# Kernel tuning notes

Measured on AMD Instinct MI355X. Metric: run time of the kernel, lower is better.

The kernel has to match this reference:

```python
import jax, jax.numpy as jnp
import numpy as np

D = 512
SCALE = float(np.sqrt(D // 8))  # sqrt(d_k), d_k = d_model/num_heads = 64
EPS = 1e-5


def _ln(x, g, b):
    m = jnp.mean(x, axis=-1, keepdims=True)
    v = jnp.var(x, axis=-1, keepdims=True)
    return (x - m) * jax.lax.rsqrt(v + EPS) * g + b


def setup_inputs() -> dict:
    key = jax.random.key(0)
    ks = jax.random.split(key, 12)
    B, S = 512, 512
    w = lambda k, shp: jax.random.normal(k, shp, dtype=jnp.float32) * 0.02
    return {
        "sentiment_vec": jax.random.normal(ks[0], (B, D), dtype=jnp.float32),
        "price_sequence": jax.random.normal(ks[1], (B, S, D), dtype=jnp.float32),
        "Wq": w(ks[2], (D, D)), "bq": jnp.zeros((D,), jnp.float32),
        "Wk": w(ks[3], (D, D)), "bk": jnp.zeros((D,), jnp.float32),
        "Wv": w(ks[4], (D, D)), "bv": jnp.zeros((D,), jnp.float32),
        "Wo": w(ks[5], (D, D)), "bo": jnp.zeros((D,), jnp.float32),
        "Wg": w(ks[6], (2 * D, D)), "bg": jnp.zeros((D,), jnp.float32),
        "g_q": jnp.ones((D,), jnp.float32), "beta_q": jnp.zeros((D,), jnp.float32),
        "g_kv": jnp.ones((D,), jnp.float32), "beta_kv": jnp.zeros((D,), jnp.float32),
    }


def reference(sentiment_vec, price_sequence, Wq, bq, Wk, bk, Wv, bv, Wo, bo,
              Wg, bg, g_q, beta_q, g_kv, beta_kv):
    # LayerNorms (query is a single token per batch element)
    Q = _ln(sentiment_vec, g_q, beta_q)            # [B, D]
    KV = _ln(price_sequence, g_kv, beta_kv)        # [B, S, D]
    # Projections (note: forward never splits heads -> single-head attention)
    q = Q @ Wq + bq                                # [B, D]
    k = KV @ Wk + bk                               # [B, S, D]
    v = KV @ Wv + bv                               # [B, S, D]
    # Single-query attention
    scores = jnp.einsum('bd,bsd->bs', q, k) / SCALE
    attn = jax.nn.softmax(scores, axis=-1)         # [B, S] (dropout: eval mode)
    ctx = jnp.einsum('bs,bsd->bd', attn, v)        # [B, D]
    ctx = ctx @ Wo + bo
    # Sigmoid gate over concat([sentiment, context])
    gate_in = jnp.concatenate([sentiment_vec, ctx], axis=-1)  # [B, 2D]
    alpha = jax.nn.sigmoid(gate_in @ Wg + bg)
    fused = alpha * ctx + (1.0 - alpha) * sentiment_vec
    return fused, attn
```

## Files before the change

kernel.cpp:

```cpp
#include <hip/hip_runtime.h>

#define NB 512
#define NS 512
#define ND 512
#define INV_SCALE 0.125f
#define LN_EPS 1e-5f

typedef __attribute__((ext_vector_type(8))) short short8;
typedef __attribute__((ext_vector_type(4))) short short4v;
typedef __attribute__((ext_vector_type(4))) float float4v;

static __device__ __forceinline__ unsigned short f2bf(float x) {
    unsigned int u = __float_as_uint(x);
    unsigned int r = (u + 0x7fffu + ((u >> 16) & 1u)) >> 16;
    return (unsigned short)r;
}
static __device__ __forceinline__ float bf2f(unsigned short h) {
    return __uint_as_float(((unsigned int)h) << 16);
}

__global__ __launch_bounds__(256) void prep_k(
    const float* __restrict__ Wq, const float* __restrict__ Wk,
    const float* __restrict__ bq, const float* __restrict__ bk,
    const float* __restrict__ bv, const float* __restrict__ Wo,
    const float* __restrict__ bo,
    float* __restrict__ Wqk, float* __restrict__ wv,
    float* __restrict__ bqk, float* __restrict__ bvo, float* __restrict__ c0) {
    const int bid = blockIdx.x;
    const int t = threadIdx.x;
    const int wave = t >> 6, lane = t & 63;

    if (bid < 256) {
        constexpr int LDK = 40;
        __shared__ __align__(16) unsigned short Ah[32 * LDK];
        __shared__ __align__(16) unsigned short Al[32 * LDK];
        __shared__ __align__(16) unsigned short Bh[32 * LDK];
        __shared__ __align__(16) unsigned short Bl[32 * LDK];
        const int m0 = (bid >> 4) * 32, n0 = (bid & 15) * 32;
        const int wm = (wave & 1) * 16, wn = (wave >> 1) * 16;
        float4v acc = (float4v){0.f, 0.f, 0.f, 0.f};
        const int arow = wm + (lane & 15);
        const int brow = wn + (lane & 15);
        const int kq8 = (lane >> 4) * 8;
        const int srow = t >> 3, skq = (t & 7) * 4;

        float4 va = *(const float4*)(Wq + (size_t)(m0 + srow) * 512 + skq);
        float4 vb = *(const float4*)(Wk + (size_t)(n0 + srow) * 512 + skq);
        for (int k0 = 0; k0 < 512; k0 += 32) {
            {
                unsigned short h0 = f2bf(va.x), h1 = f2bf(va.y), h2 = f2bf(va.z), h3 = f2bf(va.w);
                short4v hv = {(short)h0, (short)h1, (short)h2, (short)h3};
                short4v lv = {(short)f2bf(va.x - bf2f(h0)), (short)f2bf(va.y - bf2f(h1)),
                              (short)f2bf(va.z - bf2f(h2)), (short)f2bf(va.w - bf2f(h3))};
                *(short4v*)&Ah[srow * LDK + skq] = hv;
                *(short4v*)&Al[srow * LDK + skq] = lv;
            }
            {
                unsigned short h0 = f2bf(vb.x), h1 = f2bf(vb.y), h2 = f2bf(vb.z), h3 = f2bf(vb.w);
                short4v hv = {(short)h0, (short)h1, (short)h2, (short)h3};
                short4v lv = {(short)f2bf(vb.x - bf2f(h0)), (short)f2bf(vb.y - bf2f(h1)),
                              (short)f2bf(vb.z - bf2f(h2)), (short)f2bf(vb.w - bf2f(h3))};
                *(short4v*)&Bh[srow * LDK + skq] = hv;
                *(short4v*)&Bl[srow * LDK + skq] = lv;
            }
            float4 va2, vb2;
            if (k0 + 32 < 512) {
                va2 = *(const float4*)(Wq + (size_t)(m0 + srow) * 512 + k0 + 32 + skq);
                vb2 = *(const float4*)(Wk + (size_t)(n0 + srow) * 512 + k0 + 32 + skq);
            } else { va2 = va; vb2 = vb; }
            __syncthreads();
            short8 ah = *(const short8*)&Ah[arow * LDK + kq8];
            short8 al = *(const short8*)&Al[arow * LDK + kq8];
            short8 bh = *(const short8*)&Bh[brow * LDK + kq8];
            short8 bl = *(const short8*)&Bl[brow * LDK + kq8];
            acc = __builtin_amdgcn_mfma_f32_16x16x32_bf16(ah, bh, acc, 0, 0, 0);
            acc = __builtin_amdgcn_mfma_f32_16x16x32_bf16(ah, bl, acc, 0, 0, 0);
            acc = __builtin_amdgcn_mfma_f32_16x16x32_bf16(al, bh, acc, 0, 0, 0);
            __syncthreads();
            va = va2; vb = vb2;
        }
        const int coln = lane & 15, rbase = (lane >> 4) * 4;
        const int n = n0 + wn + coln;
#pragma unroll
        for (int r = 0; r < 4; ++r)
            Wqk[(size_t)(m0 + wm + rbase + r) * 512 + n] = acc[r];
    } else if (bid == 256) {
        float4 k0v = *(const float4*)(bk + 4 * lane);
        float4 k1v = *(const float4*)(bk + 256 + 4 * lane);
        for (int m = wave; m < 512; m += 4) {
            const float* r = Wq + (size_t)m * 512;
            float4 a0 = *(const float4*)(r + 4 * lane);
            float4 a1 = *(const float4*)(r + 256 + 4 * lane);
            float d = a0.x * k0v.x + a0.y * k0v.y + a0.z * k0v.z + a0.w * k0v.w +
                      a1.x * k1v.x + a1.y * k1v.y + a1.z * k1v.z + a1.w * k1v.w;
            for (int off = 32; off; off >>= 1) d += __shfl_xor(d, off, 64);
            if (lane == 0) wv[m] = d;
        }
    } else if (bid == 257) {
        float4 q0v = *(const float4*)(bq + 4 * lane);
        float4 q1v = *(const float4*)(bq + 256 + 4 * lane);
        for (int n = wave; n < 512; n += 4) {
            const float* r = Wk + (size_t)n * 512;
            float4 a0 = *(const float4*)(r + 4 * lane);
            float4 a1 = *(const float4*)(r + 256 + 4 * lane);
            float d = a0.x * q0v.x + a0.y * q0v.y + a0.z * q0v.z + a0.w * q0v.w +
                      a1.x * q1v.x + a1.y * q1v.y + a1.z * q1v.z + a1.w * q1v.w;
            for (int off = 32; off; off >>= 1) d += __shfl_xor(d, off, 64);
            if (lane == 0) bqk[n] = d;
        }
        if (wave == 0) {
            float4 b0v = *(const float4*)(bk + 4 * lane);
            float4 b1v = *(const float4*)(bk + 256 + 4 * lane);
            float d = b0v.x * q0v.x + b0v.y * q0v.y + b0v.z * q0v.z + b0v.w * q0v.w +
                      b1v.x * q1v.x + b1v.y * q1v.y + b1v.z * q1v.z + b1v.w * q1v.w;
            for (int off = 32; off; off >>= 1) d += __shfl_xor(d, off, 64);
            if (lane == 0) c0[0] = d;
        }
    } else {
        float a0 = 0.f, a1 = 0.f;
#pragma unroll 4
        for (int k = 0; k < 512; ++k) {
            float s = bv[k];
            a0 = fmaf(s, Wo[(size_t)k * 512 + t], a0);
            a1 = fmaf(s, Wo[(size_t)k * 512 + 256 + t], a1);
        }
        bvo[t] = a0 + bo[t];
        bvo[t + 256] = a1 + bo[t + 256];
    }
}

__global__ __launch_bounds__(64) void ln_s0_k(const float* __restrict__ x,
                                              const float* __restrict__ g,
                                              const float* __restrict__ be,
                                              const float* __restrict__ wv,
                                              const float* __restrict__ c0,
                                              float* __restrict__ y,
                                              float* __restrict__ s0) {
    const int row = blockIdx.x;
    const int lane = threadIdx.x;
    const float* xr = x + (size_t)row * ND;
    float4 x0 = *(const float4*)(xr + 4 * lane);
    float4 x1 = *(const float4*)(xr + 256 + 4 * lane);
    float s1 = x0.x + x0.y + x0.z + x0.w + x1.x + x1.y + x1.z + x1.w;
    float s2 = x0.x * x0.x + x0.y * x0.y + x0.z * x0.z + x0.w * x0.w +
               x1.x * x1.x + x1.y * x1.y + x1.z * x1.z + x1.w * x1.w;
    for (int off = 32; off; off >>= 1) {
        s1 += __shfl_xor(s1, off, 64);
        s2 += __shfl_xor(s2, off, 64);
    }
    float mean = s1 * (1.f / 512.f);
    float rstd = rsqrtf(s2 * (1.f / 512.f) - mean * mean + LN_EPS);
    float4 g0 = *(const float4*)(g + 4 * lane);
    float4 g1 = *(const float4*)(g + 256 + 4 * lane);
    float4 b0 = *(const float4*)(be + 4 * lane);
    float4 b1 = *(const float4*)(be + 256 + 4 * lane);
    float4 y0, y1;
    y0.x = (x0.x - mean) * rstd * g0.x + b0.x;
    y0.y = (x0.y - mean) * rstd * g0.y + b0.y;
    y0.z = (x0.z - mean) * rstd * g0.z + b0.z;
    y0.w = (x0.w - mean) * rstd * g0.w + b0.w;
    y1.x = (x1.x - mean) * rstd * g1.x + b1.x;
    y1.y = (x1.y - mean) * rstd * g1.y + b1.y;
    y1.z = (x1.z - mean) * rstd * g1.z + b1.z;
    y1.w = (x1.w - mean) * rstd * g1.w + b1.w;
    float* yr = y + (size_t)row * ND;
    *(float4*)(yr + 4 * lane) = y0;
    *(float4*)(yr + 256 + 4 * lane) = y1;
    float4 w0 = *(const float4*)(wv + 4 * lane);
    float4 w1 = *(const float4*)(wv + 256 + 4 * lane);
    float d = y0.x * w0.x + y0.y * w0.y + y0.z * w0.z + y0.w * w0.w +
              y1.x * w1.x + y1.y * w1.y + y1.z * w1.z + y1.w * w1.w;
    for (int off = 32; off; off >>= 1) d += __shfl_xor(d, off, 64);
    if (lane == 0) s0[row] = d + c0[0];
}

template <int EPI>
__global__ __launch_bounds__(256) void gemm32_k(
    const float* __restrict__ A, const float* __restrict__ B,
    const float* __restrict__ bias, float* __restrict__ C, int N, int K,
    const float* __restrict__ e_ctx, const float* __restrict__ e_sent,
    const float* __restrict__ e_add) {
    constexpr int LDK = 40;
    __shared__ __align__(16) unsigned short Ah[32 * LDK];
    __shared__ __align__(16) unsigned short Al[32 * LDK];
    __shared__ __align__(16) unsigned short Bh[32 * LDK];
    __shared__ __align__(16) unsigned short Bl[32 * LDK];
    const int t = threadIdx.x;
    const int wave = t >> 6, lane = t & 63;
    const int m0 = blockIdx.y * 32, n0 = blockIdx.x * 32;
    const int wm = (wave & 1) * 16, wn = (wave >> 1) * 16;

    float4v acc = (float4v){0.f, 0.f, 0.f, 0.f};
    const int arow = wm + (lane & 15);
    const int brow = wn + (lane & 15);
    const int kq8 = (lane >> 4) * 8;
    const int srow = t >> 3, skq = (t & 7) * 4;

    float4 va = *(const float4*)(A + (size_t)(m0 + srow) * K + skq);
    float4 vb = *(const float4*)(B + (size_t)srow * N + n0 + skq);

    for (int k0 = 0; k0 < K; k0 += 32) {
        {
            unsigned short h0 = f2bf(va.x), h1 = f2bf(va.y), h2 = f2bf(va.z), h3 = f2bf(va.w);
            short4v hv = {(short)h0, (short)h1, (short)h2, (short)h3};
            short4v lv = {(short)f2bf(va.x - bf2f(h0)), (short)f2bf(va.y - bf2f(h1)),
                          (short)f2bf(va.z - bf2f(h2)), (short)f2bf(va.w - bf2f(h3))};
            *(short4v*)&Ah[srow * LDK + skq] = hv;
            *(short4v*)&Al[srow * LDK + skq] = lv;
        }
        {
            float vv[4] = {vb.x, vb.y, vb.z, vb.w};
#pragma unroll
            for (int j = 0; j < 4; ++j) {
                unsigned short hh = f2bf(vv[j]);
                Bh[(skq + j) * LDK + srow] = hh;
                Bl[(skq + j) * LDK + srow] = f2bf(vv[j] - bf2f(hh));
            }
        }
        float4 va2, vb2;
        if (k0 + 32 < K) {
            va2 = *(const float4*)(A + (size_t)(m0 + srow) * K + k0 + 32 + skq);
            vb2 = *(const float4*)(B + (size_t)(k0 + 32 + srow) * N + n0 + skq);
        } else { va2 = va; vb2 = vb; }
        __syncthreads();
        short8 ah = *(const short8*)&Ah[arow * LDK + kq8];
        short8 al = *(const short8*)&Al[arow * LDK + kq8];
        short8 bh = *(const short8*)&Bh[brow * LDK + kq8];
        short8 bl = *(const short8*)&Bl[brow * LDK + kq8];
        acc = __builtin_amdgcn_mfma_f32_16x16x32_bf16(ah, bh, acc, 0, 0, 0);
        acc = __builtin_amdgcn_mfma_f32_16x16x32_bf16(ah, bl, acc, 0, 0, 0);
        acc = __builtin_amdgcn_mfma_f32_16x16x32_bf16(al, bh, acc, 0, 0, 0);
        __syncthreads();
        va = va2; vb = vb2;
    }

    const int coln = lane & 15, rbase = (lane >> 4) * 4;
    const int n = n0 + wn + coln;
    const float bvv = bias ? bias[n] : 0.f;
#pragma unroll
    for (int r = 0; r < 4; ++r) {
        int m = m0 + wm + rbase + r;
        float val = acc[r] + bvv;
        if (EPI == 2) {
            float z = val + e_add[(size_t)m * N + n];
            float a = 1.f / (1.f + __expf(-z));
            float cx = e_ctx[(size_t)m * N + n];
            float sv = e_sent[(size_t)m * N + n];
            val = a * cx + (1.f - a) * sv;
        }
        C[(size_t)m * N + n] = val;
    }
}

__global__ __launch_bounds__(512) void flash_fused_k(
    const float* __restrict__ ps, const float* __restrict__ g,
    const float* __restrict__ be, const float* __restrict__ qp,
    const float* __restrict__ s0v, float* __restrict__ ctx_pre,
    float* __restrict__ attn,
    const float* __restrict__ Wv, const float* __restrict__ Wo,
    float* __restrict__ Wvo,
    const float* __restrict__ sent, const float* __restrict__ Wg,
    const float* __restrict__ bg, float* __restrict__ sentg) {
    union SMemU {
        struct { float zbuf[NS]; float ubuf[8][ND]; float lw[8]; float tw[8]; } fl;
        struct { unsigned short Ah[64 * 40]; unsigned short Al[64 * 40];
                 unsigned short Bh[32 * 40]; unsigned short Bl[32 * 40]; } gm;
    };
    __shared__ __align__(16) SMemU sm;
    const int bid = blockIdx.x;
    const int t = threadIdx.x;
    const int wave = t >> 6, lane = t & 63;

    if (bid < 512) {
        const int b = bid;
        const float* qb = qp + (size_t)b * ND;
        float4 q0 = *(const float4*)(qb + 4 * lane);
        float4 q1 = *(const float4*)(qb + 256 + 4 * lane);
        float4 g0 = *(const float4*)(g + 4 * lane);
        float4 g1 = *(const float4*)(g + 256 + 4 * lane);
        float4 b0 = *(const float4*)(be + 4 * lane);
        float4 b1 = *(const float4*)(be + 256 + 4 * lane);

        float4 qg0, qg1;
        qg0.x = g0.x * q0.x; qg0.y = g0.y * q0.y; qg0.z = g0.z * q0.z; qg0.w = g0.w * q0.w;
        qg1.x = g1.x * q1.x; qg1.y = g1.y * q1.y; qg1.z = g1.z * q1.z; qg1.w = g1.w * q1.w;
        float c1 = qg0.x + qg0.y + qg0.z + qg0.w + qg1.x + qg1.y + qg1.z + qg1.w;
        float c2 = b0.x * q0.x + b0.y * q0.y + b0.z * q0.z + b0.w * q0.w +
                   b1.x * q1.x + b1.y * q1.y + b1.z * q1.z + b1.w * q1.w;
        for (int off = 32; off; off >>= 1) {
            c1 += __shfl_xor(c1, off, 64);
            c2 += __shfl_xor(c2, off, 64);
        }
        const float K2 = INV_SCALE * (c2 + s0v[b]);
        const float C1 = c1;

        float l = 0.f, t1 = 0.f;
        float4 u0 = {0.f, 0.f, 0.f, 0.f}, u1 = {0.f, 0.f, 0.f, 0.f};

        const float* base = ps + ((size_t)b * NS + wave * 64) * ND + 4 * lane;
        float4 xa0 = *(const float4*)(base);
        float4 xa1 = *(const float4*)(base + 256);
        float4 xb0 = *(const float4*)(base + ND);
        float4 xb1 = *(const float4*)(base + ND + 256);

        for (int r = 0; r < 64; r += 2) {
            float4 ya0, ya1, yb0, yb1;
            if (r < 62) {
                const float* nb = base + (size_t)(r + 2) * ND;
                ya0 = *(const float4*)(nb);
                ya1 = *(const float4*)(nb + 256);
                yb0 = *(const float4*)(nb + ND);
                yb1 = *(const float4*)(nb + ND + 256);
            } else {
                ya0 = xa0; ya1 = xa1; yb0 = xb0; yb1 = xb1;
            }
            float sa1 = xa0.x + xa0.y + xa0.z + xa0.w + xa1.x + xa1.y + xa1.z + xa1.w;
            float sb1 = xb0.x + xb0.y + xb0.z + xb0.w + xb1.x + xb1.y + xb1.z + xb1.w;
            float sa2 = xa0.x * xa0.x + xa0.y * xa0.y + xa0.z * xa0.z + xa0.w * xa0.w +
                        xa1.x * xa1.x + xa1.y * xa1.y + xa1.z * xa1.z + xa1.w * xa1.w;
            float sb2 = xb0.x * xb0.x + xb0.y * xb0.y + xb0.z * xb0.z + xb0.w * xb0.w +
                        xb1.x * xb1.x + xb1.y * xb1.y + xb1.z * xb1.z + xb1.w * xb1.w;
            float sa3 = xa0.x * qg0.x + xa0.y * qg0.y + xa0.z * qg0.z + xa0.w * qg0.w +
                        xa1.x * qg1.x + xa1.y * qg1.y + xa1.z * qg1.z + xa1.w * qg1.w;
            float sb3 = xb0.x * qg0.x + xb0.y * qg0.y + xb0.z * qg0.z + xb0.w * qg0.w +
                        xb1.x * qg1.x + xb1.y * qg1.y + xb1.z * qg1.z + xb1.w * qg1.w;
            for (int off = 32; off; off >>= 1) {
                sa1 += __shfl_xor(sa1, off, 64);
                sb1 += __shfl_xor(sb1, off, 64);
                sa2 += __shfl_xor(sa2, off, 64);
                sb2 += __shfl_xor(sb2, off, 64);
                sa3 += __shfl_xor(sa3, off, 64);
                sb3 += __shfl_xor(sb3, off, 64);
            }
            float meana = sa1 * (1.f / 512.f), meanb = sb1 * (1.f / 512.f);
            float rstda = rsqrtf(sa2 * (1.f / 512.f) - meana * meana + LN_EPS);
            float rstdb = rsqrtf(sb2 * (1.f / 512.f) - meanb * meanb + LN_EPS);
            float za = INV_SCALE * rstda * (sa3 - meana * C1) + K2;
            float zb = INV_SCALE * rstdb * (sb3 - meanb * C1) + K2;
            float pa = __expf(za), pb = __expf(zb);
            l += pa + pb;
            float pra = pa * rstda, prb = pb * rstdb;
            t1 += pra * meana + prb * meanb;
            u0.x += pra * xa0.x + prb * xb0.x;
            u0.y += pra * xa0.y + prb * xb0.y;
            u0.z += pra * xa0.z + prb * xb0.z;
            u0.w += pra * xa0.w + prb * xb0.w;
            u1.x += pra * xa1.x + prb * xb1.x;
            u1.y += pra * xa1.y + prb * xb1.y;
            u1.z += pra * xa1.z + prb * xb1.z;
            u1.w += pra * xa1.w + prb * xb1.w;
            if (lane == 0) {
                sm.fl.zbuf[wave * 64 + r] = za;
                sm.fl.zbuf[wave * 64 + r + 1] = zb;
            }
            xa0 = ya0; xa1 = ya1; xb0 = yb0; xb1 = yb1;
        }

        *(float4*)&sm.fl.ubuf[wave][4 * lane] = u0;
        *(float4*)&sm.fl.ubuf[wave][256 + 4 * lane] = u1;
        if (lane == 0) { sm.fl.lw[wave] = l; sm.fl.tw[wave] = t1; }
        __syncthreads();

        float U = 0.f;
#pragma unroll
        for (int w = 0; w < 8; ++w) U += sm.fl.ubuf[w][t];
        float L = 0.f, T = 0.f;
#pragma unroll
        for (int w = 0; w < 8; ++w) { L += sm.fl.lw[w]; T += sm.fl.tw[w]; }
        float invL = 1.f / L;
        ctx_pre[(size_t)b * ND + t] = g[t] * (U - T) * invL + be[t];
        attn[(size_t)b * NS + t] = __expf(sm.fl.zbuf[t]) * invL;
    } else {
        constexpr int LDK = 40;
        int gb = bid - 512;
        const float* A; const float* B; const float* bias; float* C;
        if (gb < 128) { A = Wv; B = Wo; bias = nullptr; C = Wvo; }
        else { gb -= 128; A = sent; B = Wg; bias = bg; C = sentg; }
        const int m0 = (gb >> 4) * 64, n0 = (gb & 15) * 32;
        const int wm = (wave & 3) * 16, wn = (wave >> 2) * 16;
        float4v acc = (float4v){0.f, 0.f, 0.f, 0.f};
        const int arow = wm + (lane & 15);
        const int brow = wn + (lane & 15);
        const int kq8 = (lane >> 4) * 8;
        const int srow = t >> 3, skq = (t & 7) * 4;
        unsigned short* Ah = sm.gm.Ah;
        unsigned short* Al = sm.gm.Al;
        unsigned short* Bh = sm.gm.Bh;
        unsigned short* Bl = sm.gm.Bl;

        float4 va = *(const float4*)(A + (size_t)(m0 + srow) * 512 + skq);
        float4 vb = {0.f, 0.f, 0.f, 0.f};
        const int bkrow = t >> 3, bnq = (t & 7) * 4;
        if (t < 256) vb = *(const float4*)(B + (size_t)bkrow * 512 + n0 + bnq);

        for (int k0 = 0; k0 < 512; k0 += 32) {
            {
                unsigned short h0 = f2bf(va.x), h1 = f2bf(va.y), h2 = f2bf(va.z), h3 = f2bf(va.w);
                short4v hv = {(short)h0, (short)h1, (short)h2, (short)h3};
                short4v lv = {(short)f2bf(va.x - bf2f(h0)), (short)f2bf(va.y - bf2f(h1)),
                              (short)f2bf(va.z - bf2f(h2)), (short)f2bf(va.w - bf2f(h3))};
                *(short4v*)&Ah[srow * LDK + skq] = hv;
                *(short4v*)&Al[srow * LDK + skq] = lv;
            }
            if (t < 256) {
                float vv[4] = {vb.x, vb.y, vb.z, vb.w};
#pragma unroll
                for (int j = 0; j < 4; ++j) {
                    unsigned short hh = f2bf(vv[j]);
                    Bh[(bnq + j) * LDK + bkrow] = hh;
                    Bl[(bnq + j) * LDK + bkrow] = f2bf(vv[j] - bf2f(hh));
                }
            }
            float4 va2 = va, vb2 = vb;
            if (k0 + 32 < 512) {
                va2 = *(const float4*)(A + (size_t)(m0 + srow) * 512 + k0 + 32 + skq);
                if (t < 256) vb2 = *(const float4*)(B + (size_t)(k0 + 32 + bkrow) * 512 + n0 + bnq);
            }
            __syncthreads();
            short8 ah = *(const short8*)&Ah[arow * LDK + kq8];
            short8 al = *(const short8*)&Al[arow * LDK + kq8];
            short8 bh = *(const short8*)&Bh[brow * LDK + kq8];
            short8 bl = *(const short8*)&Bl[brow * LDK + kq8];
            acc = __builtin_amdgcn_mfma_f32_16x16x32_bf16(ah, bh, acc, 0, 0, 0);
            acc = __builtin_amdgcn_mfma_f32_16x16x32_bf16(ah, bl, acc, 0, 0, 0);
            acc = __builtin_amdgcn_mfma_f32_16x16x32_bf16(al, bh, acc, 0, 0, 0);
            __syncthreads();
            va = va2; vb = vb2;
        }
        const int coln = lane & 15, rbase = (lane >> 4) * 4;
        const int n = n0 + wn + coln;
        const float bvv = bias ? bias[n] : 0.f;
#pragma unroll
        for (int r = 0; r < 4; ++r)
            C[(size_t)(m0 + wm + rbase + r) * 512 + n] = acc[r] + bvv;
    }
}

extern "C" void kernel_launch(void* const* d_in, const int* in_sizes, int n_in,
                              void* d_out, int out_size, void* d_ws, size_t ws_size,
                              hipStream_t stream) {
    const float* sent = (const float*)d_in[0];
    const float* ps   = (const float*)d_in[1];
    const float* Wq = (const float*)d_in[2];
    const float* bq = (const float*)d_in[3];
    const float* Wk = (const float*)d_in[4];
    const float* bk = (const float*)d_in[5];
    const float* Wv = (const float*)d_in[6];
    const float* bv = (const float*)d_in[7];
    const float* Wo = (const float*)d_in[8];
    const float* bo = (const float*)d_in[9];
    const float* Wg = (const float*)d_in[10];
    const float* bg = (const float*)d_in[11];
    const float* g_q = (const float*)d_in[12];
    const float* beta_q = (const float*)d_in[13];
    const float* g_kv = (const float*)d_in[14];
    const float* beta_kv = (const float*)d_in[15];

    float* out = (float*)d_out;
    float* attn = out + NB * ND;

    float* ws = (float*)d_ws;
    float* Wqk     = ws;
    float* Qln     = ws + 262144;
    float* qprime  = ws + 524288;
    float* ctx_pre = ws + 786432;
    float* Wvo     = ws + 1048576;
    float* sentg   = ws + 1310720;
    float* ctx2    = ws + 1572864;
    float* wv      = ws + 1835008;
    float* bqk     = ws + 1835520;
    float* bvo     = ws + 1836032;
    float* s0      = ws + 1836544;
    float* c0      = ws + 1837056;

    dim3 g32(16, 16);

    prep_k<<<259, 256, 0, stream>>>(Wq, Wk, bq, bk, bv, Wo, bo,
                                    Wqk, wv, bqk, bvo, c0);
    ln_s0_k<<<NB, 64, 0, stream>>>(sent, g_q, beta_q, wv, c0, Qln, s0);
    gemm32_k<0><<<g32, 256, 0, stream>>>(Qln, Wqk, bqk, qprime, 512, 512,
                                         nullptr, nullptr, nullptr);
    flash_fused_k<<<768, 512, 0, stream>>>(ps, g_kv, beta_kv, qprime, s0,
                                           ctx_pre, attn, Wv, Wo, Wvo,
                                           sent, Wg, bg, sentg);
    gemm32_k<0><<<g32, 256, 0, stream>>>(ctx_pre, Wvo, bvo, ctx2, 512, 512,
                                         nullptr, nullptr, nullptr);
    gemm32_k<2><<<g32, 256, 0, stream>>>(ctx2, Wg + 512 * 512, nullptr, out,
                                         512, 512, ctx2, sent, sentg);
}
```

Baseline: 817.2 us.

## Spread prep bias dot products over more blocks and unfuse side GEMMs from flash

The bias-projection dot products in prep_k, previously serialized on single blocks (bid 256/257/258), are now spread over 24 blocks so one block does not dominate the prep tail. The Wv·Wo and sent·Wg GEMMs that were co-scheduled as extra blocks inside the flash kernel are moved into separate gemm32_k launches before the flash kernel. The flash kernel becomes a pure attention kernel without the shared-memory union. This trades two extra launches for shorter critical paths and a simpler flash kernel, but loses the overlap of those GEMMs with attention.

After: 835.7 us. +2.3%, slower.

```diff
diff --git a/kernel.cpp b/kernel.cpp
--- a/kernel.cpp
+++ b/kernel.cpp
@@ -17,6 +17,16 @@
 }
 static __device__ __forceinline__ float bf2f(unsigned short h) {
     return __uint_as_float(((unsigned int)h) << 16);
+}
+
+static __device__ __forceinline__ float dot512(const float* __restrict__ x,
+                                               float4 w0, float4 w1, int lane) {
+    float4 a0 = *(const float4*)(x + 4 * lane);
+    float4 a1 = *(const float4*)(x + 256 + 4 * lane);
+    float d = a0.x * w0.x + a0.y * w0.y + a0.z * w0.z + a0.w * w0.w +
+              a1.x * w1.x + a1.y * w1.y + a1.z * w1.z + a1.w * w1.w;
+    for (int off = 32; off; off >>= 1) d += __shfl_xor(d, off, 64);
+    return d;
 }
 
 __global__ __launch_bounds__(256) void prep_k(
@@ -84,48 +94,38 @@
 #pragma unroll
         for (int r = 0; r < 4; ++r)
             Wqk[(size_t)(m0 + wm + rbase + r) * 512 + n] = acc[r];
-    } else if (bid == 256) {
-        float4 k0v = *(const float4*)(bk + 4 * lane);
-        float4 k1v = *(const float4*)(bk + 256 + 4 * lane);
-        for (int m = wave; m < 512; m += 4) {
-            const float* r = Wq + (size_t)m * 512;
-            float4 a0 = *(const float4*)(r + 4 * lane);
-            float4 a1 = *(const float4*)(r + 256 + 4 * lane);
-            float d = a0.x * k0v.x + a0.y * k0v.y + a0.z * k0v.z + a0.w * k0v.w +
-                      a1.x * k1v.x + a1.y * k1v.y + a1.z * k1v.z + a1.w * k1v.w;
-            for (int off = 32; off; off >>= 1) d += __shfl_xor(d, off, 64);
+    } else if (bid < 264) {
+        const int gb = bid - 256;
+        float4 w0 = *(const float4*)(bk + 4 * lane);
+        float4 w1 = *(const float4*)(bk + 256 + 4 * lane);
+        for (int i = 0; i < 16; ++i) {
+            int m = gb * 64 + wave * 16 + i;
+            float d = dot512(Wq + (size_t)m * 512, w0, w1, lane);
             if (lane == 0) wv[m] = d;
         }
-    } else if (bid == 257) {
-        float4 q0v = *(const float4*)(bq + 4 * lane);
-        float4 q1v = *(const float4*)(bq + 256 + 4 * lane);
-        for (int n = wave; n < 512; n += 4) {
-            const float* r = Wk + (size_t)n * 512;
-            float4 a0 = *(const float4*)(r + 4 * lane);
-            float4 a1 = *(const float4*)(r + 256 + 4 * lane);
-            float d = a0.x * q0v.x + a0.y * q0v.y + a0.z * q0v.z + a0.w * q0v.w +
-                      a1.x * q1v.x + a1.y * q1v.y + a1.z * q1v.z + a1.w * q1v.w;
-            for (int off = 32; off; off >>= 1) d += __shfl_xor(d, off, 64);
+    } else if (bid < 272) {
+        const int gb = bid - 264;
+        float4 w0 = *(const float4*)(bq + 4 * lane);
+        float4 w1 = *(const float4*)(bq + 256 + 4 * lane);
+        for (int i = 0; i < 16; ++i) {
+            int n = gb * 64 + wave * 16 + i;
+            float d = dot512(Wk + (size_t)n * 512, w0, w1, lane);
             if (lane == 0) bqk[n] = d;
         }
-        if (wave == 0) {
-            float4 b0v = *(const float4*)(bk + 4 * lane);
-            float4 b1v = *(const float4*)(bk + 256 + 4 * lane);
-            float d = b0v.x * q0v.x + b0v.y * q0v.y + b0v.z * q0v.z + b0v.w * q0v.w +
-                      b1v.x * q1v.x + b1v.y * q1v.y + b1v.z * q1v.z + b1v.w * q1v.w;
-            for (int off = 32; off; off >>= 1) d += __shfl_xor(d, off, 64);
+        if (gb == 0 && wave == 0) {
+            float d = dot512(bk, w0, w1, lane);
             if (lane == 0) c0[0] = d;
         }
     } else {
-        float a0 = 0.f, a1 = 0.f;
+        const int gb = bid - 272;
+        if (t < 64) {
+            int n = gb * 64 + t;
+            float a = 0.f;
 #pragma unroll 4
-        for (int k = 0; k < 512; ++k) {
-            float s = bv[k];
-            a0 = fmaf(s, Wo[(size_t)k * 512 + t], a0);
-            a1 = fmaf(s, Wo[(size_t)k * 512 + 256 + t], a1);
-        }
-        bvo[t] = a0 + bo[t];
-        bvo[t + 256] = a1 + bo[t + 256];
+            for (int k = 0; k < 512; ++k)
+                a = fmaf(bv[k], Wo[(size_t)k * 512 + n], a);
+            bvo[n] = a + bo[n];
+        }
     }
 }
 
@@ -252,188 +252,117 @@
     }
 }
 
-__global__ __launch_bounds__(512) void flash_fused_k(
-    const float* __restrict__ ps, const float* __restrict__ g,
-    const float* __restrict__ be, const float* __restrict__ qp,
-    const float* __restrict__ s0v, float* __restrict__ ctx_pre,
-    float* __restrict__ attn,
-    const float* __restrict__ Wv, const float* __restrict__ Wo,
-    float* __restrict__ Wvo,
-    const float* __restrict__ sent, const float* __restrict__ Wg,
-    const float* __restrict__ bg, float* __restrict__ sentg) {
-    union SMemU {
-        struct { float zbuf[NS]; float ubuf[8][ND]; float lw[8]; float tw[8]; } fl;
-        struct { unsigned short Ah[64 * 40]; unsigned short Al[64 * 40];
-                 unsigned short Bh[32 * 40]; unsigned short Bl[32 * 40]; } gm;
-    };
-    __shared__ __align__(16) SMemU sm;
-    const int bid = blockIdx.x;
+__global__ __launch_bounds__(512) void flash_k(const float* __restrict__ ps,
+                                               const float* __restrict__ g,
+                                               const float* __restrict__ be,
+                                               const float* __restrict__ qp,
+                                               const float* __restrict__ s0v,
+                                               float* __restrict__ ctx_pre,
+                                               float* __restrict__ attn) {
+    const int b = blockIdx.x;
     const int t = threadIdx.x;
     const int wave = t >> 6, lane = t & 63;
-
-    if (bid < 512) {
-        const int b = bid;
-        const float* qb = qp + (size_t)b * ND;
-        float4 q0 = *(const float4*)(qb + 4 * lane);
-        float4 q1 = *(const float4*)(qb + 256 + 4 * lane);
-        float4 g0 = *(const float4*)(g + 4 * lane);
-        float4 g1 = *(const float4*)(g + 256 + 4 * lane);
-        float4 b0 = *(const float4*)(be + 4 * lane);
-        float4 b1 = *(const float4*)(be + 256 + 4 * lane);
-
-        float4 qg0, qg1;
-        qg0.x = g0.x * q0.x; qg0.y = g0.y * q0.y; qg0.z = g0.z * q0.z; qg0.w = g0.w * q0.w;
-        qg1.x = g1.x * q1.x; qg1.y = g1.y * q1.y; qg1.z = g1.z * q1.z; qg1.w = g1.w * q1.w;
-        float c1 = qg0.x + qg0.y + qg0.z + qg0.w + qg1.x + qg1.y + qg1.z + qg1.w;
-        float c2 = b0.x * q0.x + b0.y * q0.y + b0.z * q0.z + b0.w * q0.w +
-                   b1.x * q1.x + b1.y * q1.y + b1.z * q1.z + b1.w * q1.w;
+    __shared__ float zbuf[NS];
+    __shared__ float ubuf[8][ND];
+    __shared__ float lw[8], tw[8];
+
+    const float* qb = qp + (size_t)b * ND;
+    float4 q0 = *(const float4*)(qb + 4 * lane);
+    float4 q1 = *(const float4*)(qb + 256 + 4 * lane);
+    float4 g0 = *(const float4*)(g + 4 * lane);
+    float4 g1 = *(const float4*)(g + 256 + 4 * lane);
+    float4 b0 = *(const float4*)(be + 4 * lane);
+    float4 b1 = *(const float4*)(be + 256 + 4 * lane);
+
+    float4 qg0, qg1;
+    qg0.x = g0.x * q0.x; qg0.y = g0.y * q0.y; qg0.z = g0.z * q0.z; qg0.w = g0.w * q0.w;
+    qg1.x = g1.x * q1.x; qg1.y = g1.y * q1.y; qg1.z = g1.z * q1.z; qg1.w = g1.w * q1.w;
+    float c1 = qg0.x + qg0.y + qg0.z + qg0.w + qg1.x + qg1.y + qg1.z + qg1.w;
+    float c2 = b0.x * q0.x + b0.y * q0.y + b0.z * q0.z + b0.w * q0.w +
+               b1.x * q1.x + b1.y * q1.y + b1.z * q1.z + b1.w * q1.w;
+    for (int off = 32; off; off >>= 1) {
+        c1 += __shfl_xor(c1, off, 64);
+        c2 += __shfl_xor(c2, off, 64);
+    }
+    const float K2 = INV_SCALE * (c2 + s0v[b]);
+    const float C1 = c1;
+
+    float l = 0.f, t1 = 0.f;
+    float4 u0 = {0.f, 0.f, 0.f, 0.f}, u1 = {0.f, 0.f, 0.f, 0.f};
+
+    const float* base = ps + ((size_t)b * NS + wave * 64) * ND + 4 * lane;
+    float4 xa0 = *(const float4*)(base);
+    float4 xa1 = *(const float4*)(base + 256);
+    float4 xb0 = *(const float4*)(base + ND);
+    float4 xb1 = *(const float4*)(base + ND + 256);
+
+    for (int r = 0; r < 64; r += 2) {
+        float4 ya0, ya1, yb0, yb1;
+        if (r < 62) {
+            const float* nb = base + (size_t)(r + 2) * ND;
+            ya0 = *(const float4*)(nb);
+            ya1 = *(const float4*)(nb + 256);
+            yb0 = *(const float4*)(nb + ND);
+            yb1 = *(const float4*)(nb + ND + 256);
+        } else {
+            ya0 = xa0; ya1 = xa1; yb0 = xb0; yb1 = xb1;
+        }
+        float sa1 = xa0.x + xa0.y + xa0.z + xa0.w + xa1.x + xa1.y + xa1.z + xa1.w;
+        float sb1 = xb0.x + xb0.y + xb0.z + xb0.w + xb1.x + xb1.y + xb1.z + xb1.w;
+        float sa2 = xa0.x * xa0.x + xa0.y * xa0.y + xa0.z * xa0.z + xa0.w * xa0.w +
+                    xa1.x * xa1.x + xa1.y * xa1.y + xa1.z * xa1.z + xa1.w * xa1.w;
+        float sb2 = xb0.x * xb0.x + xb0.y * xb0.y + xb0.z * xb0.z + xb0.w * xb0.w +
+                    xb1.x * xb1.x + xb1.y * xb1.y + xb1.z * xb1.z + xb1.w * xb1.w;
+        float sa3 = xa0.x * qg0.x + xa0.y * qg0.y + xa0.z * qg0.z + xa0.w * qg0.w +
+                    xa1.x * qg1.x + xa1.y * qg1.y + xa1.z * qg1.z + xa1.w * qg1.w;
+        float sb3 = xb0.x * qg0.x + xb0.y * qg0.y + xb0.z * qg0.z + xb0.w * qg0.w +
+                    xb1.x * qg1.x + xb1.y * qg1.y + xb1.z * qg1.z + xb1.w * qg1.w;
         for (int off = 32; off; off >>= 1) {
-            c1 += __shfl_xor(c1, off, 64);
-            c2 += __shfl_xor(c2, off, 64);
-        }
-        const float K2 = INV_SCALE * (c2 + s0v[b]);
-        const float C1 = c1;
-
-        float l = 0.f, t1 = 0.f;
-        float4 u0 = {0.f, 0.f, 0.f, 0.f}, u1 = {0.f, 0.f, 0.f, 0.f};
-
-        const float* base = ps + ((size_t)b * NS + wave * 64) * ND + 4 * lane;
-        float4 xa0 = *(const float4*)(base);
-        float4 xa1 = *(const float4*)(base + 256);
-        float4 xb0 = *(const float4*)(base + ND);
-        float4 xb1 = *(const float4*)(base + ND + 256);
-
-        for (int r = 0; r < 64; r += 2) {
-            float4 ya0, ya1, yb0, yb1;
-            if (r < 62) {
-                const float* nb = base + (size_t)(r + 2) * ND;
-                ya0 = *(const float4*)(nb);
-                ya1 = *(const float4*)(nb + 256);
-                yb0 = *(const float4*)(nb + ND);
-                yb1 = *(const float4*)(nb + ND + 256);
-            } else {
-                ya0 = xa0; ya1 = xa1; yb0 = xb0; yb1 = xb1;
-            }
-            float sa1 = xa0.x + xa0.y + xa0.z + xa0.w + xa1.x + xa1.y + xa1.z + xa1.w;
-            float sb1 = xb0.x + xb0.y + xb0.z + xb0.w + xb1.x + xb1.y + xb1.z + xb1.w;
-            float sa2 = xa0.x * xa0.x + xa0.y * xa0.y + xa0.z * xa0.z + xa0.w * xa0.w +
-                        xa1.x * xa1.x + xa1.y * xa1.y + xa1.z * xa1.z + xa1.w * xa1.w;
-            float sb2 = xb0.x * xb0.x + xb0.y * xb0.y + xb0.z * xb0.z + xb0.w * xb0.w +
-                        xb1.x * xb1.x + xb1.y * xb1.y + xb1.z * xb1.z + xb1.w * xb1.w;
-            float sa3 = xa0.x * qg0.x + xa0.y * qg0.y + xa0.z * qg0.z + xa0.w * qg0.w +
-                        xa1.x * qg1.x + xa1.y * qg1.y + xa1.z * qg1.z + xa1.w * qg1.w;
-            float sb3 = xb0.x * qg0.x + xb0.y * qg0.y + xb0.z * qg0.z + xb0.w * qg0.w +
-                        xb1.x * qg1.x + xb1.y * qg1.y + xb1.z * qg1.z + xb1.w * qg1.w;
-            for (int off = 32; off; off >>= 1) {
-                sa1 += __shfl_xor(sa1, off, 64);
-                sb1 += __shfl_xor(sb1, off, 64);
-                sa2 += __shfl_xor(sa2, off, 64);
-                sb2 += __shfl_xor(sb2, off, 64);
-                sa3 += __shfl_xor(sa3, off, 64);
-                sb3 += __shfl_xor(sb3, off, 64);
-            }
-            float meana = sa1 * (1.f / 512.f), meanb = sb1 * (1.f / 512.f);
-            float rstda = rsqrtf(sa2 * (1.f / 512.f) - meana * meana + LN_EPS);
-            float rstdb = rsqrtf(sb2 * (1.f / 512.f) - meanb * meanb + LN_EPS);
-            float za = INV_SCALE * rstda * (sa3 - meana * C1) + K2;
-            float zb = INV_SCALE * rstdb * (sb3 - meanb * C1) + K2;
-            float pa = __expf(za), pb = __expf(zb);
-            l += pa + pb;
-            float pra = pa * rstda, prb = pb * rstdb;
-            t1 += pra * meana + prb * meanb;
-            u0.x += pra * xa0.x + prb * xb0.x;
-            u0.y += pra * xa0.y + prb * xb0.y;
-            u0.z += pra * xa0.z + prb * xb0.z;
-            u0.w += pra * xa0.w + prb * xb0.w;
-            u1.x += pra * xa1.x + prb * xb1.x;
-            u1.y += pra * xa1.y + prb * xb1.y;
-            u1.z += pra * xa1.z + prb * xb1.z;
-            u1.w += pra * xa1.w + prb * xb1.w;
-            if (lane == 0) {
-                sm.fl.zbuf[wave * 64 + r] = za;
-                sm.fl.zbuf[wave * 64 + r + 1] = zb;
-            }
-            xa0 = ya0; xa1 = ya1; xb0 = yb0; xb1 = yb1;
-        }
-
-        *(float4*)&sm.fl.ubuf[wave][4 * lane] = u0;
-        *(float4*)&sm.fl.ubuf[wave][256 + 4 * lane] = u1;
-        if (lane == 0) { sm.fl.lw[wave] = l; sm.fl.tw[wave] = t1; }
-        __syncthreads();
-
-        float U = 0.f;
+            sa1 += __shfl_xor(sa1, off, 64);
+            sb1 += __shfl_xor(sb1, off, 64);
+            sa2 += __shfl_xor(sa2, off, 64);
+            sb2 += __shfl_xor(sb2, off, 64);
+            sa3 += __shfl_xor(sa3, off, 64);
+            sb3 += __shfl_xor(sb3, off, 64);
+        }
+        float meana = sa1 * (1.f / 512.f), meanb = sb1 * (1.f / 512.f);
+        float rstda = rsqrtf(sa2 * (1.f / 512.f) - meana * meana + LN_EPS);
+        float rstdb = rsqrtf(sb2 * (1.f / 512.f) - meanb * meanb + LN_EPS);
+        float za = INV_SCALE * rstda * (sa3 - meana * C1) + K2;
+        float zb = INV_SCALE * rstdb * (sb3 - meanb * C1) + K2;
+        float pa = __expf(za), pb = __expf(zb);
+        l += pa + pb;
+        float pra = pa * rstda, prb = pb * rstdb;
+        t1 += pra * meana + prb * meanb;
+        u0.x += pra * xa0.x + prb * xb0.x;
+        u0.y += pra * xa0.y + prb * xb0.y;
+        u0.z += pra * xa0.z + prb * xb0.z;
+        u0.w += pra * xa0.w + prb * xb0.w;
+        u1.x += pra * xa1.x + prb * xb1.x;
+        u1.y += pra * xa1.y + prb * xb1.y;
+        u1.z += pra * xa1.z + prb * xb1.z;
+        u1.w += pra * xa1.w + prb * xb1.w;
+        if (lane == 0) {
+            zbuf[wave * 64 + r] = za;
+            zbuf[wave * 64 + r + 1] = zb;
+        }
+        xa0 = ya0; xa1 = ya1; xb0 = yb0; xb1 = yb1;
+    }
+
+    *(float4*)&ubuf[wave][4 * lane] = u0;
+    *(float4*)&ubuf[wave][256 + 4 * lane] = u1;
+    if (lane == 0) { lw[wave] = l; tw[wave] = t1; }
+    __syncthreads();
+
+    float U = 0.f;
 #pragma unroll
-        for (int w = 0; w < 8; ++w) U += sm.fl.ubuf[w][t];
-        float L = 0.f, T = 0.f;
+    for (int w = 0; w < 8; ++w) U += ubuf[w][t];
+    float L = 0.f, T = 0.f;
 #pragma unroll
-        for (int w = 0; w < 8; ++w) { L += sm.fl.lw[w]; T += sm.fl.tw[w]; }
-        float invL = 1.f / L;
-        ctx_pre[(size_t)b * ND + t] = g[t] * (U - T) * invL + be[t];
-        attn[(size_t)b * NS + t] = __expf(sm.fl.zbuf[t]) * invL;
-    } else {
-        constexpr int LDK = 40;
-        int gb = bid - 512;
-        const float* A; const float* B; const float* bias; float* C;
-        if (gb < 128) { A = Wv; B = Wo; bias = nullptr; C = Wvo; }
-        else { gb -= 128; A = sent; B = Wg; bias = bg; C = sentg; }
-        const int m0 = (gb >> 4) * 64, n0 = (gb & 15) * 32;
-        const int wm = (wave & 3) * 16, wn = (wave >> 2) * 16;
-        float4v acc = (float4v){0.f, 0.f, 0.f, 0.f};
-        const int arow = wm + (lane & 15);
-        const int brow = wn + (lane & 15);
-        const int kq8 = (lane >> 4) * 8;
-        const int srow = t >> 3, skq = (t & 7) * 4;
-        unsigned short* Ah = sm.gm.Ah;
-        unsigned short* Al = sm.gm.Al;
-        unsigned short* Bh = sm.gm.Bh;
-        unsigned short* Bl = sm.gm.Bl;
-
-        float4 va = *(const float4*)(A + (size_t)(m0 + srow) * 512 + skq);
-        float4 vb = {0.f, 0.f, 0.f, 0.f};
-        const int bkrow = t >> 3, bnq = (t & 7) * 4;
-        if (t < 256) vb = *(const float4*)(B + (size_t)bkrow * 512 + n0 + bnq);
-
-        for (int k0 = 0; k0 < 512; k0 += 32) {
-            {
-                unsigned short h0 = f2bf(va.x), h1 = f2bf(va.y), h2 = f2bf(va.z), h3 = f2bf(va.w);
-                short4v hv = {(short)h0, (short)h1, (short)h2, (short)h3};
-                short4v lv = {(short)f2bf(va.x - bf2f(h0)), (short)f2bf(va.y - bf2f(h1)),
-                              (short)f2bf(va.z - bf2f(h2)), (short)f2bf(va.w - bf2f(h3))};
-                *(short4v*)&Ah[srow * LDK + skq] = hv;
-                *(short4v*)&Al[srow * LDK + skq] = lv;
-            }
-            if (t < 256) {
-                float vv[4] = {vb.x, vb.y, vb.z, vb.w};
-#pragma unroll
-                for (int j = 0; j < 4; ++j) {
-                    unsigned short hh = f2bf(vv[j]);
-                    Bh[(bnq + j) * LDK + bkrow] = hh;
-                    Bl[(bnq + j) * LDK + bkrow] = f2bf(vv[j] - bf2f(hh));
-                }
-            }
-            float4 va2 = va, vb2 = vb;
-            if (k0 + 32 < 512) {
-                va2 = *(const float4*)(A + (size_t)(m0 + srow) * 512 + k0 + 32 + skq);
-                if (t < 256) vb2 = *(const float4*)(B + (size_t)(k0 + 32 + bkrow) * 512 + n0 + bnq);
-            }
-            __syncthreads();
-            short8 ah = *(const short8*)&Ah[arow * LDK + kq8];
-            short8 al = *(const short8*)&Al[arow * LDK + kq8];
-            short8 bh = *(const short8*)&Bh[brow * LDK + kq8];
-            short8 bl = *(const short8*)&Bl[brow * LDK + kq8];
-            acc = __builtin_amdgcn_mfma_f32_16x16x32_bf16(ah, bh, acc, 0, 0, 0);
-            acc = __builtin_amdgcn_mfma_f32_16x16x32_bf16(ah, bl, acc, 0, 0, 0);
-            acc = __builtin_amdgcn_mfma_f32_16x16x32_bf16(al, bh, acc, 0, 0, 0);
-            __syncthreads();
-            va = va2; vb = vb2;
-        }
-        const int coln = lane & 15, rbase = (lane >> 4) * 4;
-        const int n = n0 + wn + coln;
-        const float bvv = bias ? bias[n] : 0.f;
-#pragma unroll
-        for (int r = 0; r < 4; ++r)
-            C[(size_t)(m0 + wm + rbase + r) * 512 + n] = acc[r] + bvv;
-    }
+    for (int w = 0; w < 8; ++w) { L += lw[w]; T += tw[w]; }
+    float invL = 1.f / L;
+    ctx_pre[(size_t)b * ND + t] = g[t] * (U - T) * invL + be[t];
+    attn[(size_t)b * NS + t] = __expf(zbuf[t]) * invL;
 }
 
 extern "C" void kernel_launch(void* const* d_in, const int* in_sizes, int n_in,
@@ -461,11 +390,11 @@
 
     float* ws = (float*)d_ws;
     float* Wqk     = ws;
-    float* Qln     = ws + 262144;
-    float* qprime  = ws + 524288;
-    float* ctx_pre = ws + 786432;
-    float* Wvo     = ws + 1048576;
-    float* sentg   = ws + 1310720;
+    float* Wvo     = ws + 262144;
+    float* sentg   = ws + 524288;
+    float* Qln     = ws + 786432;
+    float* qprime  = ws + 1048576;
+    float* ctx_pre = ws + 1310720;
     float* ctx2    = ws + 1572864;
     float* wv      = ws + 1835008;
     float* bqk     = ws + 1835520;
@@ -475,14 +404,16 @@
 
     dim3 g32(16, 16);
 
-    prep_k<<<259, 256, 0, stream>>>(Wq, Wk, bq, bk, bv, Wo, bo,
+    prep_k<<<280, 256, 0, stream>>>(Wq, Wk, bq, bk, bv, Wo, bo,
                                     Wqk, wv, bqk, bvo, c0);
+    gemm32_k<0><<<g32, 256, 0, stream>>>(Wv, Wo, nullptr, Wvo, 512, 512,
+                                         nullptr, nullptr, nullptr);
+    gemm32_k<0><<<g32, 256, 0, stream>>>(sent, Wg, bg, sentg, 512, 512,
+                                         nullptr, nullptr, nullptr);
     ln_s0_k<<<NB, 64, 0, stream>>>(sent, g_q, beta_q, wv, c0, Qln, s0);
     gemm32_k<0><<<g32, 256, 0, stream>>>(Qln, Wqk, bqk, qprime, 512, 512,
                                          nullptr, nullptr, nullptr);
-    flash_fused_k<<<768, 512, 0, stream>>>(ps, g_kv, beta_kv, qprime, s0,
-                                           ctx_pre, attn, Wv, Wo, Wvo,
-                                           sent, Wg, bg, sentg);
+    flash_k<<<NB, 512, 0, stream>>>(ps, g_kv, beta_kv, qprime, s0, ctx_pre, attn);
     gemm32_k<0><<<g32, 256, 0, stream>>>(ctx_pre, Wvo, bvo, ctx2, 512, 512,
                                          nullptr, nullptr, nullptr);
     gemm32_k<2><<<g32, 256, 0, stream>>>(ctx2, Wg + 512 * 512, nullptr, out,
```
